# Performance work log

Hardware: AMD Instinct MI355X
Metric: run time of the kernel (lower is better)

The kernel has to match this reference:

```python
import jax, jax.numpy as jnp
import numpy as np

TEMP = 0.3
EPS = 1e-09
EPS2 = 1e-10


def _unit(v):
    return v / jnp.linalg.norm(v, axis=-1, keepdims=True)


def setup_inputs() -> dict:
    key = jax.random.key(0)
    k1, k2 = jax.random.split(key)
    T, Q, D, K = 512, 8, 64, 16  # tracks, queries/track, embed dim, detections/track
    x = _unit(jax.random.normal(k1, (T * K, D), dtype=jnp.float32))
    y = _unit(jax.random.normal(k2, (T, Q, D), dtype=jnp.float32))
    track_idxs = jnp.repeat(jnp.arange(T, dtype=jnp.int64), K)  # every track id present
    return {"x": x, "track_idxs": track_idxs, "y": y}


def reference(x, track_idxs, y):
    # local_contrast=True, separate_tracks=False, static_contrast=False,
    # use_hard_condition=False, shift_to_positive=False (module defaults).
    T, Q, D = y.shape
    # All track ids 0..T-1 appear in track_idxs (by construction), so
    # ut_ids = unique(track_idxs) = arange(T) and y[ut_ids] = y.
    ut_ids = jnp.arange(T, dtype=track_idxs.dtype)
    y_flat = y.reshape(T * Q, D)          # flatten(0,1)
    y_idxs = jnp.tile(ut_ids, Q)          # ut_ids.repeat(Q) in torch semantics
    # Pairwise exp-scaled similarities: [N, T*Q]
    S = jnp.exp(jnp.einsum("nd,md->nm", x, y_flat) / TEMP)
    # Positive pairs: same track id (each x row belongs to exactly one uid),
    # so the per-uid loop collapses to one masked reduction.
    M = track_idxs[:, None] == y_idxs[None, :]
    num = jnp.sum(jnp.where(M, S, 0.0))
    den = jnp.sum(jnp.where(M, 0.0, S))
    loss = -jnp.log(num / (den + num + EPS) + EPS2)
    return loss.reshape(1)
```

## Files before the change

kernel.cpp:

```cpp
#include <hip/hip_runtime.h>
#include <hip/hip_bf16.h>

#define NROWS 8192
#define MROWS 4096
#define DDIM  64
#define TNUM  512
#define BTM   128
#define BTN   64
#define MT    4
#define GXM   (NROWS / BTM)
#define GYM   (MROWS / (BTN * MT))
#define NBLK_MAIN (GXM * GYM)
#define NPART (NBLK_MAIN * 4)
#define EXP2_SCALE 4.8089834696298780f

using bf16x8 = __attribute__((ext_vector_type(8))) short;
using f32x4  = __attribute__((ext_vector_type(4))) float;

__device__ __forceinline__ float fast_exp2(float f) {
    return __builtin_amdgcn_exp2f(f);
}
__device__ __forceinline__ short f2bf(float f) {
    __hip_bfloat16 h = __float2bfloat16(f);
    short s; __builtin_memcpy(&s, &h, 2); return s;
}

__device__ __forceinline__ int swz(int row, int colbyte) {
    return ((row << 7) + colbyte) ^ ((row & 7) << 4);
}

extern "C" __global__ __launch_bounds__(256, 4)
void ContrastiveLoss_56435870269983_kernel(
    const float* __restrict__ x, const float* __restrict__ y,
    const int* __restrict__ tid_raw,
    float2* __restrict__ part)
{
    __shared__ short xs[BTM * DDIM];
    __shared__ short ys0[BTN * DDIM];
    __shared__ short ys1[BTN * DDIM];

    const int t    = threadIdx.x;
    const int lane = t & 63;
    const int wave = t >> 6;
    const int bid  = blockIdx.x;
    const int bx   = bid & (GXM - 1);
    const int byg  = bid >> 6;

    const int n0blk  = bx * BTM;
    const int m0base = byg * (BTN * MT);

    const int n0   = (wave >> 1) * 64;
    const int m0w  = (wave & 1) * 32;
    const int rsel = lane & 15;
    const int kb   = (lane >> 4) << 4;

    const bool is64 = (tid_raw[17] != 1);
    int tia[4][4];
    #pragma unroll
    for (int i = 0; i < 4; ++i) {
        const int base = n0blk + n0 + i * 16 + (lane >> 4) * 4;
        if (!is64) {
            int4 v = *(const int4*)(tid_raw + base);
            tia[i][0] = v.x; tia[i][1] = v.y; tia[i][2] = v.z; tia[i][3] = v.w;
        } else {
            #pragma unroll
            for (int r = 0; r < 4; ++r) tia[i][r] = tid_raw[2 * (base + r)];
        }
    }

    {
        const float4* xsrc = (const float4*)(x + (size_t)n0blk * DDIM);
        #pragma unroll
        for (int q = 0; q < 8; ++q) {
            const int g = q * 256 + t;
            const int row = g >> 4, c4 = g & 15;
            float4 v = xsrc[g];
            short4 o;
            o.x = f2bf(v.x * EXP2_SCALE); o.y = f2bf(v.y * EXP2_SCALE);
            o.z = f2bf(v.z * EXP2_SCALE); o.w = f2bf(v.w * EXP2_SCALE);
            *(short4*)((char*)xs + swz(row, c4 << 3)) = o;
        }
    }
    {
        const float4* ysrc = (const float4*)(y + (size_t)m0base * DDIM);
        #pragma unroll
        for (int q = 0; q < 4; ++q) {
            const int g = q * 256 + t;
            const int row = g >> 4, c4 = g & 15;
            float4 v = ysrc[g];
            short4 o;
            o.x = f2bf(v.x); o.y = f2bf(v.y); o.z = f2bf(v.z); o.w = f2bf(v.w);
            *(short4*)((char*)ys0 + swz(row, c4 << 3)) = o;
        }
    }
    __syncthreads();

    float sa4[4] = {0.f, 0.f, 0.f, 0.f};
    float sp2[2] = {0.f, 0.f};

    #pragma unroll
    for (int mt = 0; mt < MT; ++mt) {
        short* cur = (mt & 1) ? ys1 : ys0;
        short* nxt = (mt & 1) ? ys0 : ys1;

        float4 st[4];
        if (mt + 1 < MT) {
            const float4* ysrc =
                (const float4*)(y + (size_t)(m0base + (mt + 1) * BTN) * DDIM);
            #pragma unroll
            for (int q = 0; q < 4; ++q) st[q] = ysrc[q * 256 + t];
        }

        f32x4 acc[4][2];
        #pragma unroll
        for (int i = 0; i < 4; ++i)
            #pragma unroll
            for (int j = 0; j < 2; ++j) acc[i][j] = (f32x4){0.f, 0.f, 0.f, 0.f};

        #pragma unroll
        for (int s = 0; s < 2; ++s) {
            bf16x8 af[4], bfr[2];
            #pragma unroll
            for (int i = 0; i < 4; ++i)
                af[i] = *(const bf16x8*)((const char*)xs +
                        swz(n0 + i * 16 + rsel, kb + s * 64));
            #pragma unroll
            for (int j = 0; j < 2; ++j)
                bfr[j] = *(const bf16x8*)((const char*)cur +
                         swz(m0w + j * 16 + rsel, kb + s * 64));
            #pragma unroll
            for (int i = 0; i < 4; ++i)
                #pragma unroll
                for (int j = 0; j < 2; ++j)
                    acc[i][j] = __builtin_amdgcn_mfma_f32_16x16x32_bf16(
                        af[i], bfr[j], acc[i][j], 0, 0, 0);
        }

        const int mrow = m0base + mt * BTN + m0w;
        int yc[2];
        #pragma unroll
        for (int j = 0; j < 2; ++j) yc[j] = (mrow + j * 16 + rsel) & (TNUM - 1);
        #pragma unroll
        for (int i = 0; i < 4; ++i)
            #pragma unroll
            for (int j = 0; j < 2; ++j)
                #pragma unroll
                for (int r = 0; r < 4; ++r) {
                    float e = fast_exp2(acc[i][j][r]);
                    sa4[r] += e;
                    if (tia[i][r] == yc[j]) sp2[r & 1] += e;
                }

        if (mt + 1 < MT) {
            #pragma unroll
            for (int q = 0; q < 4; ++q) {
                const int g = q * 256 + t;
                const int row = g >> 4, c4 = g & 15;
                short4 o;
                o.x = f2bf(st[q].x); o.y = f2bf(st[q].y);
                o.z = f2bf(st[q].z); o.w = f2bf(st[q].w);
                *(short4*)((char*)nxt + swz(row, c4 << 3)) = o;
            }
            __syncthreads();
        }
    }

    float sa = (sa4[0] + sa4[1]) + (sa4[2] + sa4[3]);
    float sp = sp2[0] + sp2[1];

    #pragma unroll
    for (int off = 32; off; off >>= 1) {
        sa += __shfl_down(sa, off, 64);
        sp += __shfl_down(sp, off, 64);
    }
    if (lane == 0) part[bid * 4 + wave] = make_float2(sa, sp);
}

extern "C" __global__ __launch_bounds__(256)
void cl_final_v11(const float2* __restrict__ part, unsigned int* __restrict__ out)
{
    __shared__ float red[2][256];
    const int t = threadIdx.x;
    float a = 0.0f, p = 0.0f;
    #pragma unroll
    for (int i = t; i < NPART; i += 256) {
        float2 v = part[i];
        a += v.x; p += v.y;
    }
    red[0][t] = a; red[1][t] = p;
    __syncthreads();
    for (int s = 128; s > 0; s >>= 1) {
        if (t < s) { red[0][t] += red[0][t + s]; red[1][t] += red[1][t + s]; }
        __syncthreads();
    }
    if (t == 0) {
        float total = red[0][0];
        float num   = red[1][0];
        float loss  = -__logf(num / (total + 1e-9f) + 1e-10f);
        __hip_bfloat16 bh = __float2bfloat16(loss);
        unsigned short h; __builtin_memcpy(&h, &bh, 2);
        out[0] = ((unsigned int)h << 16) | (unsigned int)h;
    }
}

extern "C" void kernel_launch(void* const* d_in, const int* in_sizes, int n_in,
                              void* d_out, int out_size, void* d_ws, size_t ws_size,
                              hipStream_t stream) {
    const float* x   = (const float*)d_in[0];
    const int*   tid = (const int*)d_in[1];
    const float* y   = (const float*)d_in[2];

    float2* part = (float2*)d_ws;
    ContrastiveLoss_56435870269983_kernel<<<NBLK_MAIN, 256, 0, stream>>>(
        x, y, tid, part);
    cl_final_v11<<<1, 256, 0, stream>>>(part, (unsigned int*)d_out);
}
```

Measured before the change: 20.47 us.

## Pre-convert inputs to bf16 in a prep kernel and stream tiles via direct global-to-LDS loads

Adds a separate prep kernel that converts x (scaled for exp2) and y to bf16 in workspace. The main kernel then fills its LDS tiles with global_load_lds 16-byte direct copies instead of load, convert and store through registers. The x tile is halved to 64 rows, doubling the grid, and A fragments are hoisted out of the m-loop. Partial sums are also reduced per block before the final kernel. The intent is to cut conversion and register-staging work and raise occupancy, at the cost of an extra kernel launch and an additional round trip through global memory for the bf16 copies.

New measurement: 22.61 us. 10.4% more time.

```diff
diff --git a/kernel.cpp b/kernel.cpp
--- a/kernel.cpp
+++ b/kernel.cpp
@@ -5,13 +5,14 @@
 #define MROWS 4096
 #define DDIM  64
 #define TNUM  512
-#define BTM   128
+#define XE    (NROWS * DDIM)
+#define YE    (MROWS * DDIM)
+#define BTM   64
 #define BTN   64
 #define MT    4
 #define GXM   (NROWS / BTM)
 #define GYM   (MROWS / (BTN * MT))
 #define NBLK_MAIN (GXM * GYM)
-#define NPART (NBLK_MAIN * 4)
 #define EXP2_SCALE 4.8089834696298780f
 
 using bf16x8 = __attribute__((ext_vector_type(8))) short;
@@ -29,36 +30,70 @@
     return ((row << 7) + colbyte) ^ ((row & 7) << 4);
 }
 
-extern "C" __global__ __launch_bounds__(256, 4)
+__device__ __forceinline__ void gload_lds16(const void* g, void* l) {
+    __builtin_amdgcn_global_load_lds(
+        (const __attribute__((address_space(1))) void*)g,
+        (__attribute__((address_space(3))) void*)l, 16, 0, 0);
+}
+
+extern "C" __global__ __launch_bounds__(256)
+void cl_prep_v12(const float* __restrict__ x, const float* __restrict__ y,
+                 short* __restrict__ xb, short* __restrict__ yb)
+{
+    const int g = blockIdx.x * 256 + threadIdx.x;
+    const int NX4 = XE / 4;
+    float4 v; short* dst; float s;
+    if (g < NX4) { v = ((const float4*)x)[g];       dst = xb + 4 * (size_t)g; s = EXP2_SCALE; }
+    else         { v = ((const float4*)y)[g - NX4]; dst = yb + 4 * (size_t)(g - NX4); s = 1.0f; }
+    short4 o;
+    o.x = f2bf(v.x * s); o.y = f2bf(v.y * s);
+    o.z = f2bf(v.z * s); o.w = f2bf(v.w * s);
+    *(short4*)dst = o;
+}
+
+extern "C" __global__ __launch_bounds__(256, 6)
 void ContrastiveLoss_56435870269983_kernel(
-    const float* __restrict__ x, const float* __restrict__ y,
-    const int* __restrict__ tid_raw,
-    float2* __restrict__ part)
+    const short* __restrict__ xb, const short* __restrict__ yb,
+    const int* __restrict__ tid_raw, float2* __restrict__ part)
 {
     __shared__ short xs[BTM * DDIM];
-    __shared__ short ys0[BTN * DDIM];
-    __shared__ short ys1[BTN * DDIM];
+    __shared__ short ys[2][BTN * DDIM];
+    __shared__ float redw[8];
 
     const int t    = threadIdx.x;
     const int lane = t & 63;
     const int wave = t >> 6;
     const int bid  = blockIdx.x;
     const int bx   = bid & (GXM - 1);
-    const int byg  = bid >> 6;
+    const int byg  = bid >> 7;
 
     const int n0blk  = bx * BTM;
     const int m0base = byg * (BTN * MT);
 
-    const int n0   = (wave >> 1) * 64;
+    const int n0w  = (wave >> 1) * 32;
     const int m0w  = (wave & 1) * 32;
     const int rsel = lane & 15;
     const int kb   = (lane >> 4) << 4;
 
+    const int lrow = lane >> 3;
+    const int lcol = ((lane & 7) ^ lrow) << 3;
+    const int soff0 = (8 * wave       + lrow) * DDIM + lcol;
+    const int soff1 = (8 * (wave + 4) + lrow) * DDIM + lcol;
+
+    {
+        const short* sx = xb + (size_t)n0blk * DDIM;
+        gload_lds16(sx + soff0, xs + wave * 512);
+        gload_lds16(sx + soff1, xs + (wave + 4) * 512);
+        const short* sy = yb + (size_t)m0base * DDIM;
+        gload_lds16(sy + soff0, ys[0] + wave * 512);
+        gload_lds16(sy + soff1, ys[0] + (wave + 4) * 512);
+    }
+
     const bool is64 = (tid_raw[17] != 1);
-    int tia[4][4];
-    #pragma unroll
-    for (int i = 0; i < 4; ++i) {
-        const int base = n0blk + n0 + i * 16 + (lane >> 4) * 4;
+    int tia[2][4];
+    #pragma unroll
+    for (int i = 0; i < 2; ++i) {
+        const int base = n0blk + n0w + i * 16 + (lane >> 4) * 4;
         if (!is64) {
             int4 v = *(const int4*)(tid_raw + base);
             tia[i][0] = v.x; tia[i][1] = v.y; tia[i][2] = v.z; tia[i][3] = v.w;
@@ -68,72 +103,48 @@
         }
     }
 
-    {
-        const float4* xsrc = (const float4*)(x + (size_t)n0blk * DDIM);
-        #pragma unroll
-        for (int q = 0; q < 8; ++q) {
-            const int g = q * 256 + t;
-            const int row = g >> 4, c4 = g & 15;
-            float4 v = xsrc[g];
-            short4 o;
-            o.x = f2bf(v.x * EXP2_SCALE); o.y = f2bf(v.y * EXP2_SCALE);
-            o.z = f2bf(v.z * EXP2_SCALE); o.w = f2bf(v.w * EXP2_SCALE);
-            *(short4*)((char*)xs + swz(row, c4 << 3)) = o;
-        }
-    }
-    {
-        const float4* ysrc = (const float4*)(y + (size_t)m0base * DDIM);
-        #pragma unroll
-        for (int q = 0; q < 4; ++q) {
-            const int g = q * 256 + t;
-            const int row = g >> 4, c4 = g & 15;
-            float4 v = ysrc[g];
-            short4 o;
-            o.x = f2bf(v.x); o.y = f2bf(v.y); o.z = f2bf(v.z); o.w = f2bf(v.w);
-            *(short4*)((char*)ys0 + swz(row, c4 << 3)) = o;
-        }
-    }
     __syncthreads();
+
+    bf16x8 af[2][2];
+    #pragma unroll
+    for (int s = 0; s < 2; ++s)
+        #pragma unroll
+        for (int i = 0; i < 2; ++i)
+            af[s][i] = *(const bf16x8*)((const char*)xs +
+                       swz(n0w + i * 16 + rsel, kb + s * 64));
 
     float sa4[4] = {0.f, 0.f, 0.f, 0.f};
     float sp2[2] = {0.f, 0.f};
 
     #pragma unroll
     for (int mt = 0; mt < MT; ++mt) {
-        short* cur = (mt & 1) ? ys1 : ys0;
-        short* nxt = (mt & 1) ? ys0 : ys1;
-
-        float4 st[4];
         if (mt + 1 < MT) {
-            const float4* ysrc =
-                (const float4*)(y + (size_t)(m0base + (mt + 1) * BTN) * DDIM);
-            #pragma unroll
-            for (int q = 0; q < 4; ++q) st[q] = ysrc[q * 256 + t];
+            const short* sy = yb + (size_t)(m0base + (mt + 1) * BTN) * DDIM;
+            short* d = ys[(mt + 1) & 1];
+            gload_lds16(sy + soff0, d + wave * 512);
+            gload_lds16(sy + soff1, d + (wave + 4) * 512);
         }
 
-        f32x4 acc[4][2];
-        #pragma unroll
-        for (int i = 0; i < 4; ++i)
+        const short* cur = ys[mt & 1];
+        f32x4 acc[2][2];
+        #pragma unroll
+        for (int i = 0; i < 2; ++i)
             #pragma unroll
             for (int j = 0; j < 2; ++j) acc[i][j] = (f32x4){0.f, 0.f, 0.f, 0.f};
 
         #pragma unroll
         for (int s = 0; s < 2; ++s) {
-            bf16x8 af[4], bfr[2];
-            #pragma unroll
-            for (int i = 0; i < 4; ++i)
-                af[i] = *(const bf16x8*)((const char*)xs +
-                        swz(n0 + i * 16 + rsel, kb + s * 64));
+            bf16x8 bfr[2];
             #pragma unroll
             for (int j = 0; j < 2; ++j)
                 bfr[j] = *(const bf16x8*)((const char*)cur +
                          swz(m0w + j * 16 + rsel, kb + s * 64));
             #pragma unroll
-            for (int i = 0; i < 4; ++i)
+            for (int i = 0; i < 2; ++i)
                 #pragma unroll
                 for (int j = 0; j < 2; ++j)
                     acc[i][j] = __builtin_amdgcn_mfma_f32_16x16x32_bf16(
-                        af[i], bfr[j], acc[i][j], 0, 0, 0);
+                        af[s][i], bfr[j], acc[i][j], 0, 0, 0);
         }
 
         const int mrow = m0base + mt * BTN + m0w;
@@ -141,7 +152,7 @@
         #pragma unroll
         for (int j = 0; j < 2; ++j) yc[j] = (mrow + j * 16 + rsel) & (TNUM - 1);
         #pragma unroll
-        for (int i = 0; i < 4; ++i)
+        for (int i = 0; i < 2; ++i)
             #pragma unroll
             for (int j = 0; j < 2; ++j)
                 #pragma unroll
@@ -151,18 +162,7 @@
                     if (tia[i][r] == yc[j]) sp2[r & 1] += e;
                 }
 
-        if (mt + 1 < MT) {
-            #pragma unroll
-            for (int q = 0; q < 4; ++q) {
-                const int g = q * 256 + t;
-                const int row = g >> 4, c4 = g & 15;
-                short4 o;
-                o.x = f2bf(st[q].x); o.y = f2bf(st[q].y);
-                o.z = f2bf(st[q].z); o.w = f2bf(st[q].w);
-                *(short4*)((char*)nxt + swz(row, c4 << 3)) = o;
-            }
-            __syncthreads();
-        }
+        __syncthreads();
     }
 
     float sa = (sa4[0] + sa4[1]) + (sa4[2] + sa4[3]);
@@ -173,17 +173,23 @@
         sa += __shfl_down(sa, off, 64);
         sp += __shfl_down(sp, off, 64);
     }
-    if (lane == 0) part[bid * 4 + wave] = make_float2(sa, sp);
+    if (lane == 0) { redw[wave] = sa; redw[4 + wave] = sp; }
+    __syncthreads();
+    if (t == 0) {
+        float A = (redw[0] + redw[1]) + (redw[2] + redw[3]);
+        float P = (redw[4] + redw[5]) + (redw[6] + redw[7]);
+        part[bid] = make_float2(A, P);
+    }
 }
 
 extern "C" __global__ __launch_bounds__(256)
-void cl_final_v11(const float2* __restrict__ part, unsigned int* __restrict__ out)
+void cl_final_v12(const float2* __restrict__ part, unsigned int* __restrict__ out)
 {
     __shared__ float red[2][256];
     const int t = threadIdx.x;
     float a = 0.0f, p = 0.0f;
     #pragma unroll
-    for (int i = t; i < NPART; i += 256) {
+    for (int i = t; i < NBLK_MAIN; i += 256) {
         float2 v = part[i];
         a += v.x; p += v.y;
     }
@@ -210,8 +216,12 @@
     const int*   tid = (const int*)d_in[1];
     const float* y   = (const float*)d_in[2];
 
-    float2* part = (float2*)d_ws;
+    short* xb = (short*)d_ws;
+    short* yb = xb + XE;
+    float2* part = (float2*)(yb + YE);
+
+    cl_prep_v12<<<(XE + YE) / 4 / 256, 256, 0, stream>>>(x, y, xb, yb);
     ContrastiveLoss_56435870269983_kernel<<<NBLK_MAIN, 256, 0, stream>>>(
-        x, y, tid, part);
-    cl_final_v11<<<1, 256, 0, stream>>>(part, (unsigned int*)d_out);
-}
+        xb, yb, tid, part);
+    cl_final_v12<<<1, 256, 0, stream>>>(part, (unsigned int*)d_out);
+}
```

## Keep x fragments in registers, halve row tile, add uniform-track fast path

Applied to the files above, without the earlier changes.

Changes block tiling from 128 x-rows and 4 y-tiles to 64 x-rows and 8 y-tiles, which doubles the grid. Each wave now loads its x fragments straight from global memory into registers as bf16, so the x shared-memory buffer and its loads are gone. A wave-uniform fast path applies when each lane's four x rows share one track id; it sums the four exps before a single mask compare. Partials are first reduced per block through shared memory, which adds a sync but shrinks the final reduction input.

Measured after the change: 20.07 us, median of 2. 2.0% less time.

```diff
diff --git a/kernel.cpp b/kernel.cpp
--- a/kernel.cpp
+++ b/kernel.cpp
@@ -5,13 +5,12 @@
 #define MROWS 4096
 #define DDIM  64
 #define TNUM  512
-#define BTM   128
+#define BTM   64
 #define BTN   64
-#define MT    4
+#define MT    8
 #define GXM   (NROWS / BTM)
 #define GYM   (MROWS / (BTN * MT))
 #define NBLK_MAIN (GXM * GYM)
-#define NPART (NBLK_MAIN * 4)
 #define EXP2_SCALE 4.8089834696298780f
 
 using bf16x8 = __attribute__((ext_vector_type(8))) short;
@@ -35,30 +34,53 @@
     const int* __restrict__ tid_raw,
     float2* __restrict__ part)
 {
-    __shared__ short xs[BTM * DDIM];
-    __shared__ short ys0[BTN * DDIM];
-    __shared__ short ys1[BTN * DDIM];
+    __shared__ short ys[2][BTN * DDIM];
+    __shared__ float redw[8];
 
     const int t    = threadIdx.x;
     const int lane = t & 63;
     const int wave = t >> 6;
     const int bid  = blockIdx.x;
     const int bx   = bid & (GXM - 1);
-    const int byg  = bid >> 6;
+    const int byg  = bid >> 7;
 
     const int n0blk  = bx * BTM;
     const int m0base = byg * (BTN * MT);
 
-    const int n0   = (wave >> 1) * 64;
-    const int m0w  = (wave & 1) * 32;
+    const int xw   = (wave >> 1) * 32;
+    const int yw   = (wave & 1) * 32;
     const int rsel = lane & 15;
-    const int kb   = (lane >> 4) << 4;
+    const int khi  = lane >> 4;
+    const int kb   = khi << 4;
+
+    const float4* ysrc0 = (const float4*)(y + (size_t)m0base * DDIM);
+    float4 sty[4];
+    #pragma unroll
+    for (int q = 0; q < 4; ++q) sty[q] = ysrc0[q * 256 + t];
+
+    bf16x8 af[2][2];
+    #pragma unroll
+    for (int i = 0; i < 2; ++i)
+        #pragma unroll
+        for (int s = 0; s < 2; ++s) {
+            const float* p = x + (size_t)(n0blk + xw + i * 16 + rsel) * DDIM
+                               + s * 32 + khi * 8;
+            float4 a0 = *(const float4*)p;
+            float4 a1 = *(const float4*)(p + 4);
+            bf16x8 f;
+            f[0] = f2bf(a0.x * EXP2_SCALE); f[1] = f2bf(a0.y * EXP2_SCALE);
+            f[2] = f2bf(a0.z * EXP2_SCALE); f[3] = f2bf(a0.w * EXP2_SCALE);
+            f[4] = f2bf(a1.x * EXP2_SCALE); f[5] = f2bf(a1.y * EXP2_SCALE);
+            f[6] = f2bf(a1.z * EXP2_SCALE); f[7] = f2bf(a1.w * EXP2_SCALE);
+            af[i][s] = f;
+        }
 
     const bool is64 = (tid_raw[17] != 1);
-    int tia[4][4];
-    #pragma unroll
-    for (int i = 0; i < 4; ++i) {
-        const int base = n0blk + n0 + i * 16 + (lane >> 4) * 4;
+    int tia[2][4];
+    bool ok = true;
+    #pragma unroll
+    for (int i = 0; i < 2; ++i) {
+        const int base = n0blk + xw + i * 16 + khi * 4;
         if (!is64) {
             int4 v = *(const int4*)(tid_raw + base);
             tia[i][0] = v.x; tia[i][1] = v.y; tia[i][2] = v.z; tia[i][3] = v.w;
@@ -66,43 +88,27 @@
             #pragma unroll
             for (int r = 0; r < 4; ++r) tia[i][r] = tid_raw[2 * (base + r)];
         }
-    }
-
-    {
-        const float4* xsrc = (const float4*)(x + (size_t)n0blk * DDIM);
-        #pragma unroll
-        for (int q = 0; q < 8; ++q) {
-            const int g = q * 256 + t;
-            const int row = g >> 4, c4 = g & 15;
-            float4 v = xsrc[g];
-            short4 o;
-            o.x = f2bf(v.x * EXP2_SCALE); o.y = f2bf(v.y * EXP2_SCALE);
-            o.z = f2bf(v.z * EXP2_SCALE); o.w = f2bf(v.w * EXP2_SCALE);
-            *(short4*)((char*)xs + swz(row, c4 << 3)) = o;
-        }
-    }
-    {
-        const float4* ysrc = (const float4*)(y + (size_t)m0base * DDIM);
-        #pragma unroll
-        for (int q = 0; q < 4; ++q) {
-            const int g = q * 256 + t;
-            const int row = g >> 4, c4 = g & 15;
-            float4 v = ysrc[g];
-            short4 o;
-            o.x = f2bf(v.x); o.y = f2bf(v.y); o.z = f2bf(v.z); o.w = f2bf(v.w);
-            *(short4*)((char*)ys0 + swz(row, c4 << 3)) = o;
-        }
+        ok = ok && (tia[i][0] == tia[i][1]) && (tia[i][1] == tia[i][2])
+                && (tia[i][2] == tia[i][3]);
+    }
+    const bool fastm = __all((int)ok);
+
+    #pragma unroll
+    for (int q = 0; q < 4; ++q) {
+        const int g = q * 256 + t;
+        const int row = g >> 4, c4 = g & 15;
+        short4 o;
+        o.x = f2bf(sty[q].x); o.y = f2bf(sty[q].y);
+        o.z = f2bf(sty[q].z); o.w = f2bf(sty[q].w);
+        *(short4*)((char*)ys[0] + swz(row, c4 << 3)) = o;
     }
     __syncthreads();
 
-    float sa4[4] = {0.f, 0.f, 0.f, 0.f};
-    float sp2[2] = {0.f, 0.f};
+    float sag[4] = {0.f, 0.f, 0.f, 0.f};
+    float spg[2] = {0.f, 0.f};
 
     #pragma unroll
     for (int mt = 0; mt < MT; ++mt) {
-        short* cur = (mt & 1) ? ys1 : ys0;
-        short* nxt = (mt & 1) ? ys0 : ys1;
-
         float4 st[4];
         if (mt + 1 < MT) {
             const float4* ysrc =
@@ -111,47 +117,60 @@
             for (int q = 0; q < 4; ++q) st[q] = ysrc[q * 256 + t];
         }
 
-        f32x4 acc[4][2];
+        const short* cur = ys[mt & 1];
+        f32x4 acc[2][2];
         #pragma unroll
-        for (int i = 0; i < 4; ++i)
+        for (int i = 0; i < 2; ++i)
             #pragma unroll
             for (int j = 0; j < 2; ++j) acc[i][j] = (f32x4){0.f, 0.f, 0.f, 0.f};
 
         #pragma unroll
         for (int s = 0; s < 2; ++s) {
-            bf16x8 af[4], bfr[2];
-            #pragma unroll
-            for (int i = 0; i < 4; ++i)
-                af[i] = *(const bf16x8*)((const char*)xs +
-                        swz(n0 + i * 16 + rsel, kb + s * 64));
+            bf16x8 bfr[2];
             #pragma unroll
             for (int j = 0; j < 2; ++j)
                 bfr[j] = *(const bf16x8*)((const char*)cur +
-                         swz(m0w + j * 16 + rsel, kb + s * 64));
-            #pragma unroll
-            for (int i = 0; i < 4; ++i)
+                         swz(yw + j * 16 + rsel, kb + s * 64));
+            #pragma unroll
+            for (int i = 0; i < 2; ++i)
                 #pragma unroll
                 for (int j = 0; j < 2; ++j)
                     acc[i][j] = __builtin_amdgcn_mfma_f32_16x16x32_bf16(
-                        af[i], bfr[j], acc[i][j], 0, 0, 0);
-        }
-
-        const int mrow = m0base + mt * BTN + m0w;
+                        af[i][s], bfr[j], acc[i][j], 0, 0, 0);
+        }
+
+        const int mrow = m0base + mt * BTN + yw;
         int yc[2];
-        #pragma unroll
-        for (int j = 0; j < 2; ++j) yc[j] = (mrow + j * 16 + rsel) & (TNUM - 1);
-        #pragma unroll
-        for (int i = 0; i < 4; ++i)
-            #pragma unroll
-            for (int j = 0; j < 2; ++j)
+        yc[0] = (mrow + rsel) & (TNUM - 1);
+        yc[1] = (mrow + 16 + rsel) & (TNUM - 1);
+        if (fastm) {
+            #pragma unroll
+            for (int i = 0; i < 2; ++i)
                 #pragma unroll
-                for (int r = 0; r < 4; ++r) {
-                    float e = fast_exp2(acc[i][j][r]);
-                    sa4[r] += e;
-                    if (tia[i][r] == yc[j]) sp2[r & 1] += e;
+                for (int j = 0; j < 2; ++j) {
+                    float e0 = fast_exp2(acc[i][j][0]);
+                    float e1 = fast_exp2(acc[i][j][1]);
+                    float e2 = fast_exp2(acc[i][j][2]);
+                    float e3 = fast_exp2(acc[i][j][3]);
+                    float g = (e0 + e1) + (e2 + e3);
+                    sag[2 * i + j] += g;
+                    if (tia[i][0] == yc[j]) spg[j] += g;
                 }
+        } else {
+            #pragma unroll
+            for (int i = 0; i < 2; ++i)
+                #pragma unroll
+                for (int j = 0; j < 2; ++j)
+                    #pragma unroll
+                    for (int r = 0; r < 4; ++r) {
+                        float e = fast_exp2(acc[i][j][r]);
+                        sag[2 * i + j] += e;
+                        if (tia[i][r] == yc[j]) spg[j] += e;
+                    }
+        }
 
         if (mt + 1 < MT) {
+            short* nxt = ys[(mt + 1) & 1];
             #pragma unroll
             for (int q = 0; q < 4; ++q) {
                 const int g = q * 256 + t;
@@ -165,25 +184,31 @@
         }
     }
 
-    float sa = (sa4[0] + sa4[1]) + (sa4[2] + sa4[3]);
-    float sp = sp2[0] + sp2[1];
+    float sa = (sag[0] + sag[1]) + (sag[2] + sag[3]);
+    float sp = spg[0] + spg[1];
 
     #pragma unroll
     for (int off = 32; off; off >>= 1) {
         sa += __shfl_down(sa, off, 64);
         sp += __shfl_down(sp, off, 64);
     }
-    if (lane == 0) part[bid * 4 + wave] = make_float2(sa, sp);
+    if (lane == 0) { redw[wave] = sa; redw[4 + wave] = sp; }
+    __syncthreads();
+    if (t == 0) {
+        float A = (redw[0] + redw[1]) + (redw[2] + redw[3]);
+        float P = (redw[4] + redw[5]) + (redw[6] + redw[7]);
+        part[bid] = make_float2(A, P);
+    }
 }
 
 extern "C" __global__ __launch_bounds__(256)
-void cl_final_v11(const float2* __restrict__ part, unsigned int* __restrict__ out)
+void cl_final_v14(const float2* __restrict__ part, unsigned int* __restrict__ out)
 {
     __shared__ float red[2][256];
     const int t = threadIdx.x;
     float a = 0.0f, p = 0.0f;
     #pragma unroll
-    for (int i = t; i < NPART; i += 256) {
+    for (int i = t; i < NBLK_MAIN; i += 256) {
         float2 v = part[i];
         a += v.x; p += v.y;
     }
@@ -213,5 +238,5 @@
     float2* part = (float2*)d_ws;
     ContrastiveLoss_56435870269983_kernel<<<NBLK_MAIN, 256, 0, stream>>>(
         x, y, tid, part);
-    cl_final_v11<<<1, 256, 0, stream>>>(part, (unsigned int*)d_out);
-}
+    cl_final_v14<<<1, 256, 0, stream>>>(part, (unsigned int*)d_out);
+}
```
